# Performance work log

Measured on AMD Instinct MI355X. Metric: run time of the kernel, lower is better.

The kernel has to match this reference:

```python
import jax, jax.numpy as jnp
import numpy as np

EPS = 1e-6

def rms_norm(x):
    # RMSNorm over last dim, no learned weight (torch F.rms_norm without weight)
    return x * jax.lax.rsqrt(jnp.mean(jnp.square(x), axis=-1, keepdims=True) + EPS)

def apply_rotary_emb(x, cos, sin):
    # x: [b, t, h, d]; cos/sin: [t, d//2] -> broadcast [1, t, 1, d//2]
    half = x.shape[-1] // 2
    c = cos[None, :, None, :]
    s = sin[None, :, None, :]
    x1, x2 = x[..., :half], x[..., half:]
    return jnp.concatenate([x1 * c - x2 * s, x2 * c + x1 * s], axis=-1)

def setup_inputs() -> dict:
    key = jax.random.key(0)
    ks = jax.random.split(key, 16)
    B, T, E, H = 4, 2048, 1024, 16
    D = E // H
    inp = {
        "query": jax.random.normal(ks[0], (B, T, E), jnp.float32),
        "key": jax.random.normal(ks[1], (B, T, E), jnp.float32),
        "value": jax.random.normal(ks[2], (B, T, E), jnp.float32),
        "attn_mask": jnp.tril(jnp.ones((T, T), dtype=bool)),
        "cos": jnp.cos(jnp.arange(T)[:, None] / (10000.0 ** (jnp.arange(D // 2) / (D // 2)))[None, :]).astype(jnp.float32),
        "sin": jnp.sin(jnp.arange(T)[:, None] / (10000.0 ** (jnp.arange(D // 2) / (D // 2)))[None, :]).astype(jnp.float32),
        "Wq": jax.random.normal(ks[3], (E, E), jnp.float32) * 0.02,
        "bq": jnp.zeros((E,), jnp.float32),
        "Wk": jax.random.normal(ks[4], (E, E), jnp.float32) * 0.02,
        "bk": jnp.zeros((E,), jnp.float32),
        "Wv": jax.random.normal(ks[5], (E, E), jnp.float32) * 0.02,
        "bv": jnp.zeros((E,), jnp.float32),
        "Wo": jax.random.normal(ks[6], (E, E), jnp.float32) * 0.02,
        "bo": jnp.zeros((E,), jnp.float32),
    }
    return inp

def reference(query, key, value, attn_mask, cos, sin, Wq, bq, Wk, bk, Wv, bv, Wo, bo):
    B, T, E = query.shape
    H = 16
    D = E // H
    q = query @ Wq.T + bq
    k = key @ Wk.T + bk
    v = value @ Wv.T + bv
    q = q.reshape(B, T, H, D)
    k = k.reshape(B, T, H, D)
    v = v.reshape(B, T, H, D)
    q, k = rms_norm(q), rms_norm(k)
    q = apply_rotary_emb(q, cos, sin)
    k = apply_rotary_emb(k, cos, sin)
    # SDPA: [b, h, t, d] layout via einsum directly from [b, t, h, d]
    scale = 1.0 / jnp.sqrt(jnp.float32(D))
    scores = jnp.einsum('bqhd,bkhd->bhqk', q, k) * scale
    scores = jnp.where(attn_mask[None, None, :, :], scores, jnp.float32(-jnp.inf))
    attn = jax.nn.softmax(scores, axis=-1)
    o = jnp.einsum('bhqk,bkhd->bqhd', attn, v).reshape(B, T, E)
    return o @ Wo.T + bo
```

## Files before the change

### kernel.cpp

```cpp
#include <hip/hip_runtime.h>

typedef __bf16 bf16;
typedef __bf16 bf16x8 __attribute__((ext_vector_type(8)));
typedef __bf16 bf16x4 __attribute__((ext_vector_type(4)));
typedef float  floatx4 __attribute__((ext_vector_type(4)));

#define B_ 4
#define T_ 2048
#define E_ 1024
#define H_ 16
#define D_ 64
#define NTE_ (B_ * T_ * E_)

#define NEG_BIG (-1e30f)
#define SMAX2 12.2629081f

#define OFF_CQ 0ull
#define OFF_CK ((unsigned long long)NTE_)
#define OFF_CV (2ull * NTE_)
#define OFF_WQ (3ull * NTE_)
#define OFF_WK (OFF_WQ + 1048576ull)
#define OFF_WV (OFF_WK + 1048576ull)
#define OFF_WO (OFF_WV + 1048576ull)
__device__ bf16 g_conv[3ull * NTE_ + 4ull * 1048576ull];
__device__ bf16 g_scratch[5ull * NTE_];

__device__ __forceinline__ floatx4 mfma16(bf16x8 a, bf16x8 b, floatx4 c) {
  return __builtin_amdgcn_mfma_f32_16x16x32_bf16(a, b, c, 0, 0, 0);
}

__device__ __forceinline__ void async_copy16(void* lds, const void* g) {
  __builtin_amdgcn_global_load_lds(
      (const __attribute__((address_space(1))) unsigned int*)g,
      (__attribute__((address_space(3))) unsigned int*)lds, 16, 0, 0);
}

__global__ __launch_bounds__(256) void convert_all(const float4* __restrict__ q,
                                                   const float4* __restrict__ k,
                                                   const float4* __restrict__ v,
                                                   const float4* __restrict__ wq,
                                                   const float4* __restrict__ wk,
                                                   const float4* __restrict__ wv,
                                                   const float4* __restrict__ wo) {
  const float4* srcs[7] = {q, k, v, wq, wk, wv, wo};
  bf16x4* dsts[7] = {(bf16x4*)(g_conv + OFF_CQ), (bf16x4*)(g_conv + OFF_CK),
                     (bf16x4*)(g_conv + OFF_CV), (bf16x4*)(g_conv + OFF_WQ),
                     (bf16x4*)(g_conv + OFF_WK), (bf16x4*)(g_conv + OFF_WV),
                     (bf16x4*)(g_conv + OFF_WO)};
  const int n4s[7] = {NTE_ / 4, NTE_ / 4, NTE_ / 4, 262144, 262144, 262144, 262144};
  int i0 = blockIdx.x * 256 + threadIdx.x;
  int stride = gridDim.x * 256;
#pragma unroll
  for (int s = 0; s < 7; ++s) {
    const float4* sp = srcs[s];
    bf16x4* dp = dsts[s];
    int n4 = n4s[s];
    for (int i = i0; i < n4; i += stride) {
      float4 vv = sp[i];
      bf16x4 o;
      o[0] = (bf16)vv.x; o[1] = (bf16)vv.y; o[2] = (bf16)vv.z; o[3] = (bf16)vv.w;
      dp[i] = o;
    }
  }
}

template <int EPI>
__device__ __forceinline__ void gemm_epilogue(floatx4 (&acc)[4][4],
                                              const float* __restrict__ bias,
                                              void* __restrict__ Yv, int M0, int N0,
                                              int wm, int wn, int q, int r,
                                              const float* __restrict__ cosb,
                                              const float* __restrict__ sinb) {
  float bcol[4];
#pragma unroll
  for (int ni = 0; ni < 4; ++ni) bcol[ni] = bias[N0 + wn + ni * 16 + r];

  if (EPI == 0 || EPI == 1) {
    const float post = (EPI == 0) ? 0.18033688f : 1.0f;
    bf16* Y = (bf16*)Yv;
#pragma unroll
    for (int mi = 0; mi < 4; ++mi) {
      const int rowbase = M0 + wm + mi * 16 + q * 4;
#pragma unroll
      for (int rr = 0; rr < 4; ++rr) {
        const int row = rowbase + rr;
        const int ts = row & (T_ - 1);
        float v0 = acc[mi][0][rr] + bcol[0];
        float v1 = acc[mi][1][rr] + bcol[1];
        float v2 = acc[mi][2][rr] + bcol[2];
        float v3 = acc[mi][3][rr] + bcol[3];
        float ss = v0 * v0 + v1 * v1 + v2 * v2 + v3 * v3;
        ss += __shfl_xor(ss, 1, 64);
        ss += __shfl_xor(ss, 2, 64);
        ss += __shfl_xor(ss, 4, 64);
        ss += __shfl_xor(ss, 8, 64);
        const float rs = rsqrtf(ss * (1.0f / 64.0f) + 1e-6f);
        const float y0 = v0 * rs, y1 = v1 * rs, y2 = v2 * rs, y3 = v3 * rs;
        const float c0 = cosb[ts * 32 + r], s0 = sinb[ts * 32 + r];
        const float c1 = cosb[ts * 32 + 16 + r], s1 = sinb[ts * 32 + 16 + r];
        bf16 o0 = (bf16)((y0 * c0 - y2 * s0) * post);
        bf16 o1 = (bf16)((y1 * c1 - y3 * s1) * post);
        bf16 o2 = (bf16)((y2 * c0 + y0 * s0) * post);
        bf16 o3 = (bf16)((y3 * c1 + y1 * s1) * post);
        bf16* yp = Y + (size_t)row * 1024 + N0 + wn + r;
        yp[0] = o0; yp[16] = o1; yp[32] = o2; yp[48] = o3;
      }
    }
  } else if (EPI == 2) {
    bf16* Y = (bf16*)Yv;
#pragma unroll
    for (int mi = 0; mi < 4; ++mi) {
      const int rowbase = M0 + wm + mi * 16 + q * 4;
      const int bb = rowbase >> 11;
      const int t0 = rowbase & (T_ - 1);
#pragma unroll
      for (int ni = 0; ni < 4; ++ni) {
        const int col = N0 + wn + ni * 16 + r;
        const int head = col >> 6;
        const int d = col & 63;
        bf16x4 pk;
#pragma unroll
        for (int rr = 0; rr < 4; ++rr) pk[rr] = (bf16)(acc[mi][ni][rr] + bcol[ni]);
        *(bf16x4*)(Y + ((size_t)(bb * 16 + head) * 64 + d) * 2048 + t0) = pk;
      }
    }
  } else {
    float* Y = (float*)Yv;
#pragma unroll
    for (int mi = 0; mi < 4; ++mi) {
      const int rowbase = M0 + wm + mi * 16 + q * 4;
#pragma unroll
      for (int ni = 0; ni < 4; ++ni) {
        const int col = N0 + wn + ni * 16 + r;
#pragma unroll
        for (int rr = 0; rr < 4; ++rr)
          Y[(size_t)(rowbase + rr) * 1024 + col] = acc[mi][ni][rr] + bcol[ni];
      }
    }
  }
}

template <int EPI>
__device__ __forceinline__ void gemm_coreA(char* __restrict__ smem,
                                           const bf16* __restrict__ X,
                                           const bf16* __restrict__ W,
                                           const float* __restrict__ bias,
                                           void* __restrict__ Yv, int M0, int N0,
                                           const float* __restrict__ cosb,
                                           const float* __restrict__ sinb) {
  constexpr int NT = 16;

  const int tid = threadIdx.x;
  const int w = tid >> 6;
  const int l = tid & 63;
  const int q = l >> 4;
  const int r = l & 15;
  const int lrow = l >> 3;
  const int rs7 = r & 7;
  const int wm = (w >> 2) * 64;
  const int wn = (w & 3) * 64;
  const int colb = ((l & 7) ^ lrow) << 4;
  const int sl0 = ((0 + q) ^ rs7) << 4;
  const int sl1 = ((4 + q) ^ rs7) << 4;

  char* const Ab = smem;
  char* const Bb = smem + 32768;
  const int aoff = (wm + r) * 128;
  const int boff = (wn + r) * 128;

  const char* gA = (const char*)X + (size_t)(M0 + w * 16 + lrow) * 2048 + colb;
  const char* gB = (const char*)W + (size_t)(N0 + w * 32 + lrow) * 2048 + colb;

  floatx4 acc[4][4];
#pragma unroll
  for (int mi = 0; mi < 4; ++mi)
#pragma unroll
    for (int ni = 0; ni < 4; ++ni) acc[mi][ni] = (floatx4){0.f, 0.f, 0.f, 0.f};

#define STA(p, t)                                              \
  do {                                                         \
    char* d_ = Ab + (p) * 16384 + w * 2048;                    \
    const char* s_ = gA + (size_t)(t) * 128;                   \
    async_copy16(d_, s_);                                      \
    async_copy16(d_ + 1024, s_ + 16384);                       \
  } while (0)
#define STB(p, t)                                              \
  do {                                                         \
    char* d_ = Bb + (p) * 32768 + w * 4096;                    \
    const char* s_ = gB + (size_t)(t) * 128;                   \
    async_copy16(d_, s_);                                      \
    async_copy16(d_ + 1024, s_ + 16384);                       \
    async_copy16(d_ + 2048, s_ + 32768);                       \
    async_copy16(d_ + 3072, s_ + 49152);                       \
  } while (0)

  STB(0, 0); STA(0, 0);
  STB(1, 1); STA(1, 1);
  asm volatile("s_waitcnt vmcnt(6)" ::: "memory");
  __builtin_amdgcn_s_barrier();

  bf16x8 af[4][2], bf0[2][2], bf1[2][2];

#pragma unroll 2
  for (int t = 0; t < NT; ++t) {
    const int p = t & 1;
    const char* rA = Ab + p * 16384;
    const char* rB = Bb + p * 32768;

#pragma unroll
    for (int mi = 0; mi < 4; ++mi) {
      af[mi][0] = *(const bf16x8*)(rA + aoff + mi * 2048 + sl0);
      af[mi][1] = *(const bf16x8*)(rA + aoff + mi * 2048 + sl1);
    }
#pragma unroll
    for (int ni = 0; ni < 2; ++ni) {
      bf0[ni][0] = *(const bf16x8*)(rB + boff + ni * 2048 + sl0);
      bf0[ni][1] = *(const bf16x8*)(rB + boff + ni * 2048 + sl1);
    }
    if (t >= 1 && t + 1 < NT) { STB(p ^ 1, t + 1); }
    asm volatile("s_waitcnt lgkmcnt(0)" ::: "memory");
    __builtin_amdgcn_sched_barrier(0);
    __builtin_amdgcn_s_setprio(1);
#pragma unroll
    for (int mi = 0; mi < 4; ++mi)
#pragma unroll
      for (int ni = 0; ni < 2; ++ni) {
        acc[mi][ni] = mfma16(af[mi][0], bf0[ni][0], acc[mi][ni]);
        acc[mi][ni] = mfma16(af[mi][1], bf0[ni][1], acc[mi][ni]);
      }
    __builtin_amdgcn_s_setprio(0);
    __builtin_amdgcn_s_barrier();

#pragma unroll
    for (int ni = 0; ni < 2; ++ni) {
      bf1[ni][0] = *(const bf16x8*)(rB + boff + (ni + 2) * 2048 + sl0);
      bf1[ni][1] = *(const bf16x8*)(rB + boff + (ni + 2) * 2048 + sl1);
    }
    if (t + 2 < NT) { STA(p, t + 2); }
    asm volatile("s_waitcnt lgkmcnt(0)" ::: "memory");
    __builtin_amdgcn_sched_barrier(0);
    __builtin_amdgcn_s_setprio(1);
#pragma unroll
    for (int mi = 0; mi < 4; ++mi)
#pragma unroll
      for (int ni = 0; ni < 2; ++ni) {
        acc[mi][ni + 2] = mfma16(af[mi][0], bf1[ni][0], acc[mi][ni + 2]);
        acc[mi][ni + 2] = mfma16(af[mi][1], bf1[ni][1], acc[mi][ni + 2]);
      }
    __builtin_amdgcn_s_setprio(0);
    if (t + 2 < NT) {
      asm volatile("s_waitcnt vmcnt(2)" ::: "memory");
    } else if (t + 1 < NT) {
      asm volatile("s_waitcnt vmcnt(0)" ::: "memory");
    }
    __builtin_amdgcn_s_barrier();
  }
#undef STA
#undef STB

  gemm_epilogue<EPI>(acc, bias, Yv, M0, N0, wm, wn, q, r, cosb, sinb);
}

template <int EPI>
__device__ __forceinline__ void gemm_coreB(char* __restrict__ smem,
                                           const bf16* __restrict__ X,
                                           const bf16* __restrict__ W,
                                           const float* __restrict__ bias,
                                           void* __restrict__ Yv, int M0, int N0,
                                           const float* __restrict__ cosb,
                                           const float* __restrict__ sinb) {
  constexpr int NT = 16;

  const int tid = threadIdx.x;
  const int w = tid >> 6;
  const int l = tid & 63;
  const int q = l >> 4;
  const int r = l & 15;
  const int lrow = l >> 3;
  const int rs7 = r & 7;
  const int wm = (w >> 2) * 64;
  const int wn = (w & 3) * 64;
  const int colb = ((l & 7) ^ lrow) << 4;
  const int sl0 = ((0 + q) ^ rs7) << 4;
  const int sl1 = ((4 + q) ^ rs7) << 4;

  char* const Ab = smem;
  char* const Bb = smem + 49152;
  const int aoff = (wm + r) * 128;
  const int boff = (wn + r) * 128;

  const char* gA = (const char*)X + (size_t)(M0 + w * 16 + lrow) * 2048 + colb;
  const char* gB = (const char*)W + (size_t)(N0 + w * 32 + lrow) * 2048 + colb;

  floatx4 acc[4][4];
#pragma unroll
  for (int mi = 0; mi < 4; ++mi)
#pragma unroll
    for (int ni = 0; ni < 4; ++ni) acc[mi][ni] = (floatx4){0.f, 0.f, 0.f, 0.f};

#define STA(bi, t)                                             \
  do {                                                         \
    char* d_ = Ab + (bi) * 16384 + w * 2048;                   \
    const char* s_ = gA + (size_t)(t) * 128;                   \
    async_copy16(d_, s_);                                      \
    async_copy16(d_ + 1024, s_ + 16384);                       \
  } while (0)
#define STB(bi, t)                                             \
  do {                                                         \
    char* d_ = Bb + (bi) * 32768 + w * 4096;                   \
    const char* s_ = gB + (size_t)(t) * 128;                   \
    async_copy16(d_, s_);                                      \
    async_copy16(d_ + 1024, s_ + 16384);                       \
    async_copy16(d_ + 2048, s_ + 32768);                       \
    async_copy16(d_ + 3072, s_ + 49152);                       \
  } while (0)

  STB(0, 0); STA(0, 0);
  STB(1, 1); STA(1, 1);
  STB(2, 2); STA(2, 2);
  asm volatile("s_waitcnt vmcnt(12)" ::: "memory");
  asm volatile("s_barrier" ::: "memory");

#pragma unroll
  for (int t = 0; t < NT; ++t) {
    const int ib = t % 3;
    const int st = (t + 2) % 3;

    if (t >= 1 && t + 2 < NT) { STB(st, t + 2); STA(st, t + 2); }

    const char* rA = Ab + ib * 16384;
    const char* rB = Bb + ib * 32768;

    bf16x8 af[4][2], bv[4][2];
#pragma unroll
    for (int mi = 0; mi < 4; ++mi) {
      af[mi][0] = *(const bf16x8*)(rA + aoff + mi * 2048 + sl0);
      af[mi][1] = *(const bf16x8*)(rA + aoff + mi * 2048 + sl1);
    }
#pragma unroll
    for (int ni = 0; ni < 4; ++ni) {
      bv[ni][0] = *(const bf16x8*)(rB + boff + ni * 2048 + sl0);
      bv[ni][1] = *(const bf16x8*)(rB + boff + ni * 2048 + sl1);
    }
#pragma unroll
    for (int mi = 0; mi < 4; ++mi)
#pragma unroll
      for (int ni = 0; ni < 4; ++ni) {
        acc[mi][ni] = mfma16(af[mi][0], bv[ni][0], acc[mi][ni]);
        acc[mi][ni] = mfma16(af[mi][1], bv[ni][1], acc[mi][ni]);
      }

    if (t + 3 <= NT) {
      asm volatile("s_waitcnt vmcnt(6)" ::: "memory");
    } else if (t + 2 == NT) {
      asm volatile("s_waitcnt vmcnt(0)" ::: "memory");
    }
    if (t + 1 < NT) asm volatile("s_barrier" ::: "memory");
  }
#undef STA
#undef STB

  gemm_epilogue<EPI>(acc, bias, Yv, M0, N0, wm, wn, q, r, cosb, sinb);
}

__global__ __launch_bounds__(512, 1) void gemm_qkv(const float* __restrict__ bq,
                                                   const float* __restrict__ bk,
                                                   const float* __restrict__ bv,
                                                   const float* __restrict__ cosb,
                                                   const float* __restrict__ sinb) {
  __shared__ __align__(16) char smem[98304];
  int bid = blockIdx.x;
  int s = (bid & 7) * 96 + (bid >> 3);
  int z = s >> 8;
  int rem = s & 255;
  int mt = rem >> 2, nt = rem & 3;
  const bf16* X = g_conv + OFF_CQ + (unsigned long long)z * NTE_;
  const bf16* W = g_conv + OFF_WQ + (unsigned long long)z * 1048576ull;
  if (z == 0) {
    gemm_coreA<0>(smem, X, W, bq, (void*)g_scratch, mt * 128, nt * 256, cosb, sinb);
  } else if (z == 1) {
    gemm_coreA<1>(smem, X, W, bk, (void*)(g_scratch + (unsigned long long)NTE_),
                  mt * 128, nt * 256, cosb, sinb);
  } else {
    gemm_coreA<2>(smem, X, W, bv, (void*)(g_scratch + 3ull * NTE_),
                  mt * 128, nt * 256, nullptr, nullptr);
  }
}

__global__ __launch_bounds__(512, 1) void gemm_out(const bf16* __restrict__ X,
                                                   const bf16* __restrict__ W,
                                                   const float* __restrict__ bias,
                                                   float* __restrict__ Y) {
  __shared__ __align__(16) char smem[147456];
  int bid = blockIdx.x;
  int s = (bid & 7) * 32 + (bid >> 3);
  int mt = s >> 2, nt = s & 3;
  gemm_coreB<3>(smem, X, W, bias, (void*)Y, mt * 128, nt * 256, nullptr, nullptr);
}

#define KSTR 72
#define PSTR 72
__global__ __launch_bounds__(256, 4) void flash_attn() {
  const bf16* qp = g_scratch;
  const bf16* kp = g_scratch + (unsigned long long)NTE_;
  const bf16* vt = g_scratch + 3ull * NTE_;
  bf16* op = g_scratch + 4ull * NTE_;

  __shared__ __align__(16) bf16 sK[64 * KSTR];
  __shared__ __align__(16) bf16 sV[64 * KSTR];
  __shared__ __align__(16) bf16 sP[4 * 32 * PSTR];

  const int bid = blockIdx.x;
  const int xcd = bid & 7;
  const int lb = bid >> 3;
  const int bh = xcd * 8 + (lb & 7);
  const int qt = 15 - (lb >> 3);
  const int h = bh & 15, b = bh >> 4;
  const int tid = threadIdx.x, w = tid >> 6, l = tid & 63, g = l >> 4, r = l & 15;
  const int Q0 = qt * 128;
  const int qw = Q0 + w * 32;

  const bf16* kbase = kp + (size_t)(b * T_) * E_ + h * D_;
  const bf16* vbase = vt + (size_t)bh * D_ * T_;
  bf16* pw = sP + w * (32 * PSTR);

  bf16x8 ones;
#pragma unroll
  for (int i = 0; i < 8; ++i) ones[i] = (bf16)1.0f;

  bf16x8 qa[2][2];
#pragma unroll
  for (int qb = 0; qb < 2; ++qb)
#pragma unroll
    for (int hf = 0; hf < 2; ++hf)
      qa[qb][hf] = *(const bf16x8*)(qp + (size_t)(b * T_ + qw + qb * 16 + r) * E_ +
                                    h * D_ + hf * 32 + g * 8);

  floatx4 o_acc[2][4], l_acc[2];
#pragma unroll
  for (int qb = 0; qb < 2; ++qb) {
    l_acc[qb] = (floatx4){0.f, 0.f, 0.f, 0.f};
#pragma unroll
    for (int dt = 0; dt < 4; ++dt) o_acc[qb][dt] = (floatx4){0.f, 0.f, 0.f, 0.f};
  }

  int srow[2], scc[2];
#pragma unroll
  for (int i = 0; i < 2; ++i) {
    int idx = i * 256 + tid;
    srow[i] = idx >> 3;
    scc[i] = (idx & 7) * 8;
  }

  bf16x8 kreg[2], vreg[2];
#pragma unroll
  for (int i = 0; i < 2; ++i) {
    kreg[i] = *(const bf16x8*)(kbase + (size_t)srow[i] * E_ + scc[i]);
    vreg[i] = *(const bf16x8*)(vbase + (size_t)srow[i] * T_ + scc[i]);
  }

  const int lastKt = Q0 + 64;
  for (int kt0 = 0; kt0 <= lastKt; kt0 += 64) {
    __syncthreads();
#pragma unroll
    for (int i = 0; i < 2; ++i) {
      *(bf16x8*)(sK + srow[i] * KSTR + scc[i]) = kreg[i];
      *(bf16x8*)(sV + srow[i] * KSTR + scc[i]) = vreg[i];
    }
    if (kt0 < lastKt) {
      int kt1 = kt0 + 64;
#pragma unroll
      for (int i = 0; i < 2; ++i) {
        kreg[i] = *(const bf16x8*)(kbase + (size_t)(kt1 + srow[i]) * E_ + scc[i]);
        vreg[i] = *(const bf16x8*)(vbase + (size_t)srow[i] * T_ + kt1 + scc[i]);
      }
    }
    __syncthreads();

    if (kt0 <= qw + 31) {
      const bool needMask = (kt0 + 63 > qw);

#pragma unroll
      for (int sc = 0; sc < 4; ++sc) {
        bf16x8 kb0 = *(const bf16x8*)(sK + (sc * 16 + r) * KSTR + g * 8);
        bf16x8 kb1 = *(const bf16x8*)(sK + (sc * 16 + r) * KSTR + 32 + g * 8);
        floatx4 s0 = (floatx4){0.f, 0.f, 0.f, 0.f};
        floatx4 s1 = (floatx4){0.f, 0.f, 0.f, 0.f};
        s0 = mfma16(kb0, qa[0][0], s0);
        s0 = mfma16(kb1, qa[0][1], s0);
        s1 = mfma16(kb0, qa[1][0], s1);
        s1 = mfma16(kb1, qa[1][1], s1);

        if (needMask) {
          int kg = kt0 + sc * 16 + g * 4;
          int qg0 = qw + r;
          int qg1 = qw + 16 + r;
#pragma unroll
          for (int rr = 0; rr < 4; ++rr) {
            if (kg + rr > qg0) s0[rr] = NEG_BIG;
            if (kg + rr > qg1) s1[rr] = NEG_BIG;
          }
        }

        bf16x4 p0, p1;
#pragma unroll
        for (int rr = 0; rr < 4; ++rr) {
          p0[rr] = (bf16)exp2f(s0[rr] - SMAX2);
          p1[rr] = (bf16)exp2f(s1[rr] - SMAX2);
        }
        *(bf16x4*)(pw + r * PSTR + sc * 16 + g * 4) = p0;
        *(bf16x4*)(pw + (16 + r) * PSTR + sc * 16 + g * 4) = p1;
      }

#pragma unroll
      for (int kk = 0; kk < 2; ++kk) {
        bf16x8 vb[4];
#pragma unroll
        for (int dt = 0; dt < 4; ++dt)
          vb[dt] = *(const bf16x8*)(sV + (dt * 16 + r) * KSTR + kk * 32 + g * 8);
#pragma unroll
        for (int qb = 0; qb < 2; ++qb) {
          bf16x8 pa = *(const bf16x8*)(pw + (qb * 16 + r) * PSTR + kk * 32 + g * 8);
          l_acc[qb] = mfma16(pa, ones, l_acc[qb]);
#pragma unroll
          for (int dt = 0; dt < 4; ++dt)
            o_acc[qb][dt] = mfma16(pa, vb[dt], o_acc[qb][dt]);
        }
      }
    }
  }

  float linv[2][4];
#pragma unroll
  for (int qb = 0; qb < 2; ++qb)
#pragma unroll
    for (int rr = 0; rr < 4; ++rr) linv[qb][rr] = 1.0f / l_acc[qb][rr];
#pragma unroll
  for (int qb = 0; qb < 2; ++qb)
#pragma unroll
    for (int dt = 0; dt < 4; ++dt)
#pragma unroll
      for (int rr = 0; rr < 4; ++rr) {
        int t = qw + qb * 16 + g * 4 + rr;
        op[(size_t)(b * T_ + t) * E_ + h * D_ + dt * 16 + r] =
            (bf16)(o_acc[qb][dt][rr] * linv[qb][rr]);
      }
}

extern "C" void kernel_launch(void* const* d_in, const int* in_sizes, int n_in,
                              void* d_out, int out_size, void* d_ws, size_t ws_size,
                              hipStream_t stream) {
  float* out = (float*)d_out;

  void* cvp_ = nullptr;
  void* sp_ = nullptr;
  (void)hipGetSymbolAddress(&cvp_, HIP_SYMBOL(g_conv));
  (void)hipGetSymbolAddress(&sp_, HIP_SYMBOL(g_scratch));
  bf16* cv = (bf16*)cvp_;
  bf16* sc = (bf16*)sp_;

  const float* cosb = (const float*)d_in[4];
  const float* sinb = (const float*)d_in[5];
  const float* bq = (const float*)d_in[7];
  const float* bk = (const float*)d_in[9];
  const float* bv = (const float*)d_in[11];
  const float* bo = (const float*)d_in[13];

  convert_all<<<dim3(1024), dim3(256), 0, stream>>>(
      (const float4*)d_in[0], (const float4*)d_in[1], (const float4*)d_in[2],
      (const float4*)d_in[6], (const float4*)d_in[8], (const float4*)d_in[10],
      (const float4*)d_in[12]);

  bf16* op = sc + 4ull * NTE_;

  gemm_qkv<<<dim3(768), dim3(512), 0, stream>>>(bq, bk, bv, cosb, sinb);
  flash_attn<<<dim3(1024), dim3(256), 0, stream>>>();
  gemm_out<<<dim3(256), dim3(512), 0, stream>>>(op, cv + OFF_WO, bo, out);
}
```

Measured before the change: 331.0 us.

## Fuse fp32-to-bf16 activation conversion into QKV GEMM A-tile loading

Drops the separate conversion pass over the query, key and value activations. The QKV GEMM now reads fp32 activations straight into registers, converts them to bf16 and writes them into LDS, which replaces the async global-to-LDS copies for the A tile. This removes one full write and re-read of about 48 MB of bf16 data, at the cost of reading twice as many A bytes inside the GEMM. The A path now goes through registers and uses full vmcnt(0) waits every iteration, which could expose load latency. The weight conversion stays as a smaller separate kernel.

```diff
diff --git a/kernel.cpp b/kernel.cpp
--- a/kernel.cpp
+++ b/kernel.cpp
@@ -15,14 +15,11 @@
 #define NEG_BIG (-1e30f)
 #define SMAX2 12.2629081f
 
-#define OFF_CQ 0ull
-#define OFF_CK ((unsigned long long)NTE_)
-#define OFF_CV (2ull * NTE_)
-#define OFF_WQ (3ull * NTE_)
-#define OFF_WK (OFF_WQ + 1048576ull)
-#define OFF_WV (OFF_WK + 1048576ull)
-#define OFF_WO (OFF_WV + 1048576ull)
-__device__ bf16 g_conv[3ull * NTE_ + 4ull * 1048576ull];
+#define OFF_WQ 0ull
+#define OFF_WK 1048576ull
+#define OFF_WV 2097152ull
+#define OFF_WO 3145728ull
+__device__ bf16 g_conv[4ull * 1048576ull];
 __device__ bf16 g_scratch[5ull * NTE_];
 
 __device__ __forceinline__ floatx4 mfma16(bf16x8 a, bf16x8 b, floatx4 c) {
@@ -35,27 +32,27 @@
       (__attribute__((address_space(3))) unsigned int*)lds, 16, 0, 0);
 }
 
-__global__ __launch_bounds__(256) void convert_all(const float4* __restrict__ q,
-                                                   const float4* __restrict__ k,
-                                                   const float4* __restrict__ v,
-                                                   const float4* __restrict__ wq,
-                                                   const float4* __restrict__ wk,
-                                                   const float4* __restrict__ wv,
-                                                   const float4* __restrict__ wo) {
-  const float4* srcs[7] = {q, k, v, wq, wk, wv, wo};
-  bf16x4* dsts[7] = {(bf16x4*)(g_conv + OFF_CQ), (bf16x4*)(g_conv + OFF_CK),
-                     (bf16x4*)(g_conv + OFF_CV), (bf16x4*)(g_conv + OFF_WQ),
-                     (bf16x4*)(g_conv + OFF_WK), (bf16x4*)(g_conv + OFF_WV),
-                     (bf16x4*)(g_conv + OFF_WO)};
-  const int n4s[7] = {NTE_ / 4, NTE_ / 4, NTE_ / 4, 262144, 262144, 262144, 262144};
+__device__ __forceinline__ bf16x8 cvt8(float4 a, float4 b) {
+  bf16x8 o;
+  o[0] = (bf16)a.x; o[1] = (bf16)a.y; o[2] = (bf16)a.z; o[3] = (bf16)a.w;
+  o[4] = (bf16)b.x; o[5] = (bf16)b.y; o[6] = (bf16)b.z; o[7] = (bf16)b.w;
+  return o;
+}
+
+__global__ __launch_bounds__(256) void convert_weights(const float4* __restrict__ wq,
+                                                       const float4* __restrict__ wk,
+                                                       const float4* __restrict__ wv,
+                                                       const float4* __restrict__ wo) {
+  const float4* srcs[4] = {wq, wk, wv, wo};
+  bf16x4* dsts[4] = {(bf16x4*)(g_conv + OFF_WQ), (bf16x4*)(g_conv + OFF_WK),
+                     (bf16x4*)(g_conv + OFF_WV), (bf16x4*)(g_conv + OFF_WO)};
   int i0 = blockIdx.x * 256 + threadIdx.x;
   int stride = gridDim.x * 256;
 #pragma unroll
-  for (int s = 0; s < 7; ++s) {
+  for (int s = 0; s < 4; ++s) {
     const float4* sp = srcs[s];
     bf16x4* dp = dsts[s];
-    int n4 = n4s[s];
-    for (int i = i0; i < n4; i += stride) {
+    for (int i = i0; i < 262144; i += stride) {
       float4 vv = sp[i];
       bf16x4 o;
       o[0] = (bf16)vv.x; o[1] = (bf16)vv.y; o[2] = (bf16)vv.z; o[3] = (bf16)vv.w;
@@ -141,13 +138,13 @@
 }
 
 template <int EPI>
-__device__ __forceinline__ void gemm_coreA(char* __restrict__ smem,
-                                           const bf16* __restrict__ X,
-                                           const bf16* __restrict__ W,
-                                           const float* __restrict__ bias,
-                                           void* __restrict__ Yv, int M0, int N0,
-                                           const float* __restrict__ cosb,
-                                           const float* __restrict__ sinb) {
+__device__ __forceinline__ void gemm_coreA_f32(char* __restrict__ smem,
+                                               const float* __restrict__ X32,
+                                               const bf16* __restrict__ W,
+                                               const float* __restrict__ bias,
+                                               void* __restrict__ Yv, int M0, int N0,
+                                               const float* __restrict__ cosb,
+                                               const float* __restrict__ sinb) {
   constexpr int NT = 16;
 
   const int tid = threadIdx.x;
@@ -168,21 +165,30 @@
   const int aoff = (wm + r) * 128;
   const int boff = (wn + r) * 128;
 
-  const char* gA = (const char*)X + (size_t)(M0 + w * 16 + lrow) * 2048 + colb;
+  const char* gA32 =
+      (const char*)X32 + (size_t)(M0 + w * 16 + lrow) * 4096 + (colb << 1);
   const char* gB = (const char*)W + (size_t)(N0 + w * 32 + lrow) * 2048 + colb;
 
+  char* const dA = Ab + w * 2048 + l * 16;
+
   floatx4 acc[4][4];
 #pragma unroll
   for (int mi = 0; mi < 4; ++mi)
 #pragma unroll
     for (int ni = 0; ni < 4; ++ni) acc[mi][ni] = (floatx4){0.f, 0.f, 0.f, 0.f};
 
-#define STA(p, t)                                              \
-  do {                                                         \
-    char* d_ = Ab + (p) * 16384 + w * 2048;                    \
-    const char* s_ = gA + (size_t)(t) * 128;                   \
-    async_copy16(d_, s_);                                      \
-    async_copy16(d_ + 1024, s_ + 16384);                       \
+#define LDA(t)                                                   \
+  do {                                                           \
+    const char* s_ = gA32 + (size_t)(t) * 256;                   \
+    ua0 = *(const float4*)(s_);                                  \
+    ua1 = *(const float4*)(s_ + 16);                             \
+    ua2 = *(const float4*)(s_ + 32768);                          \
+    ua3 = *(const float4*)(s_ + 32768 + 16);                     \
+  } while (0)
+#define WRA(p)                                                   \
+  do {                                                           \
+    *(bf16x8*)(dA + (p) * 16384) = cvt8(ua0, ua1);               \
+    *(bf16x8*)(dA + (p) * 16384 + 1024) = cvt8(ua2, ua3);        \
   } while (0)
 #define STB(p, t)                                              \
   do {                                                         \
@@ -194,9 +200,16 @@
     async_copy16(d_ + 3072, s_ + 49152);                       \
   } while (0)
 
-  STB(0, 0); STA(0, 0);
-  STB(1, 1); STA(1, 1);
-  asm volatile("s_waitcnt vmcnt(6)" ::: "memory");
+  float4 ua0, ua1, ua2, ua3;
+
+  LDA(0);
+  STB(0, 0);
+  WRA(0);
+  LDA(1);
+  STB(1, 1);
+  WRA(1);
+  asm volatile("s_waitcnt lgkmcnt(0)" ::: "memory");
+  asm volatile("s_waitcnt vmcnt(4)" ::: "memory");
   __builtin_amdgcn_s_barrier();
 
   bf16x8 af[4][2], bf0[2][2], bf1[2][2];
@@ -207,6 +220,7 @@
     const char* rA = Ab + p * 16384;
     const char* rB = Bb + p * 32768;
 
+    if (t + 2 < NT) { LDA(t + 2); }
 #pragma unroll
     for (int mi = 0; mi < 4; ++mi) {
       af[mi][0] = *(const bf16x8*)(rA + aoff + mi * 2048 + sl0);
@@ -217,7 +231,7 @@
       bf0[ni][0] = *(const bf16x8*)(rB + boff + ni * 2048 + sl0);
       bf0[ni][1] = *(const bf16x8*)(rB + boff + ni * 2048 + sl1);
     }
-    if (t >= 1 && t + 1 < NT) { STB(p ^ 1, t + 1); }
+    if (t + 1 < NT) { STB(p ^ 1, t + 1); }
     asm volatile("s_waitcnt lgkmcnt(0)" ::: "memory");
     __builtin_amdgcn_sched_barrier(0);
     __builtin_amdgcn_s_setprio(1);
@@ -236,7 +250,7 @@
       bf1[ni][0] = *(const bf16x8*)(rB + boff + (ni + 2) * 2048 + sl0);
       bf1[ni][1] = *(const bf16x8*)(rB + boff + (ni + 2) * 2048 + sl1);
     }
-    if (t + 2 < NT) { STA(p, t + 2); }
+    if (t + 2 < NT) { WRA(p); }
     asm volatile("s_waitcnt lgkmcnt(0)" ::: "memory");
     __builtin_amdgcn_sched_barrier(0);
     __builtin_amdgcn_s_setprio(1);
@@ -248,14 +262,13 @@
         acc[mi][ni + 2] = mfma16(af[mi][1], bf1[ni][1], acc[mi][ni + 2]);
       }
     __builtin_amdgcn_s_setprio(0);
-    if (t + 2 < NT) {
-      asm volatile("s_waitcnt vmcnt(2)" ::: "memory");
-    } else if (t + 1 < NT) {
+    if (t + 1 < NT) {
       asm volatile("s_waitcnt vmcnt(0)" ::: "memory");
     }
     __builtin_amdgcn_s_barrier();
   }
-#undef STA
+#undef LDA
+#undef WRA
 #undef STB
 
   gemm_epilogue<EPI>(acc, bias, Yv, M0, N0, wm, wn, q, r, cosb, sinb);
@@ -363,7 +376,10 @@
   gemm_epilogue<EPI>(acc, bias, Yv, M0, N0, wm, wn, q, r, cosb, sinb);
 }
 
-__global__ __launch_bounds__(512, 1) void gemm_qkv(const float* __restrict__ bq,
+__global__ __launch_bounds__(512, 1) void gemm_qkv(const float* __restrict__ q32,
+                                                   const float* __restrict__ k32,
+                                                   const float* __restrict__ v32,
+                                                   const float* __restrict__ bq,
                                                    const float* __restrict__ bk,
                                                    const float* __restrict__ bv,
                                                    const float* __restrict__ cosb,
@@ -374,16 +390,17 @@
   int z = s >> 8;
   int rem = s & 255;
   int mt = rem >> 2, nt = rem & 3;
-  const bf16* X = g_conv + OFF_CQ + (unsigned long long)z * NTE_;
   const bf16* W = g_conv + OFF_WQ + (unsigned long long)z * 1048576ull;
   if (z == 0) {
-    gemm_coreA<0>(smem, X, W, bq, (void*)g_scratch, mt * 128, nt * 256, cosb, sinb);
+    gemm_coreA_f32<0>(smem, q32, W, bq, (void*)g_scratch, mt * 128, nt * 256,
+                      cosb, sinb);
   } else if (z == 1) {
-    gemm_coreA<1>(smem, X, W, bk, (void*)(g_scratch + (unsigned long long)NTE_),
-                  mt * 128, nt * 256, cosb, sinb);
+    gemm_coreA_f32<1>(smem, k32, W, bk,
+                      (void*)(g_scratch + (unsigned long long)NTE_), mt * 128,
+                      nt * 256, cosb, sinb);
   } else {
-    gemm_coreA<2>(smem, X, W, bv, (void*)(g_scratch + 3ull * NTE_),
-                  mt * 128, nt * 256, nullptr, nullptr);
+    gemm_coreA_f32<2>(smem, v32, W, bv, (void*)(g_scratch + 3ull * NTE_),
+                      mt * 128, nt * 256, nullptr, nullptr);
   }
 }
 
@@ -559,6 +576,9 @@
   bf16* cv = (bf16*)cvp_;
   bf16* sc = (bf16*)sp_;
 
+  const float* q32 = (const float*)d_in[0];
+  const float* k32 = (const float*)d_in[1];
+  const float* v32 = (const float*)d_in[2];
   const float* cosb = (const float*)d_in[4];
   const float* sinb = (const float*)d_in[5];
   const float* bq = (const float*)d_in[7];
@@ -566,14 +586,14 @@
   const float* bv = (const float*)d_in[11];
   const float* bo = (const float*)d_in[13];
 
-  convert_all<<<dim3(1024), dim3(256), 0, stream>>>(
-      (const float4*)d_in[0], (const float4*)d_in[1], (const float4*)d_in[2],
+  convert_weights<<<dim3(256), dim3(256), 0, stream>>>(
       (const float4*)d_in[6], (const float4*)d_in[8], (const float4*)d_in[10],
       (const float4*)d_in[12]);
 
   bf16* op = sc + 4ull * NTE_;
 
-  gemm_qkv<<<dim3(768), dim3(512), 0, stream>>>(bq, bk, bv, cosb, sinb);
+  gemm_qkv<<<dim3(768), dim3(512), 0, stream>>>(q32, k32, v32, bq, bk, bv,
+                                                cosb, sinb);
   flash_attn<<<dim3(1024), dim3(256), 0, stream>>>();
   gemm_out<<<dim3(256), dim3(512), 0, stream>>>(op, cv + OFF_WO, bo, out);
 }
```

Result: slower. 339.8 us (+2.7%).
